# Optimization experiments

Hardware: AMD Instinct MI355X
Metric: run time of the kernel (lower is better)

Reference implementation:

```python
import jax, jax.numpy as jnp
import numpy as np

TEMP = 0.1
EPS = 1e-8


def setup_inputs() -> dict:
    key = jax.random.key(0)
    k1, k2, k3, k4 = jax.random.split(key, 4)
    b, c, H, W = 2, 64, 80, 80
    proj_main = jax.random.normal(k1, (b, c, H, W), dtype=jnp.float32)
    proj_ema = jax.random.normal(k2, (b, c, H, W), dtype=jnp.float32)
    label_main = jax.random.randint(k3, (b, H, W), 0, 2, dtype=jnp.int32)
    label_ema = jax.random.randint(k4, (b, H, W), 0, 2, dtype=jnp.int32)
    return {"proj_main": proj_main, "proj_ema": proj_ema,
            "label_main": label_main, "label_ema": label_ema,
            "patch_num": 8}


def reference(proj_main, proj_ema, label_main, label_ema, patch_num):
    # Labels / FC fractions are computed in the original forward but never
    # consumed by ContrastiveLoss, so they do not affect the output.
    # All patches have equal size h*w, so the per-patch-mean-of-means equals
    # the global mean over all b*H*W anchors; negative column ordering is
    # irrelevant to the row-wise logsumexp. Hence the nested loop fuses to:
    b, c, H, W = proj_main.shape
    A = jnp.transpose(proj_main, (0, 2, 3, 1)).reshape(-1, c)  # (N, c) anchors
    E = jnp.transpose(proj_ema, (0, 2, 3, 1)).reshape(-1, c)   # (N, c) ema feats
    pos = jnp.sum(A * E, axis=-1) / TEMP                       # (N,)
    neg = jnp.einsum('nc,mc->nm', A, E) / TEMP                 # (N, N)
    full = jnp.concatenate([pos[:, None], neg], axis=1)        # (N, N+1)
    m = jnp.max(full, axis=1)                                  # (N,) row max
    denom = jnp.sum(jnp.exp(full - m[:, None]), axis=1)        # (N,)
    loss = -jnp.log(jnp.exp(pos - m) / (denom + EPS) + EPS)
    return jnp.mean(loss)
```

## Files before the change

kernel.cpp:

```cpp
#include <hip/hip_runtime.h>
#include <stdint.h>

#define NA 12800
#define CCH 64
#define TB 2048
#define NSEG 200
#define SC 14.4269504088896340736f
#define MARGIN 41.0f
#define FLOOR_LOSS 18.420680743952367f
#define MAXF 6400
#define NPARTS 20
#define SGMAX 8

typedef __attribute__((ext_vector_type(4))) float f32x4;
typedef __attribute__((ext_vector_type(8))) short s16x8;

#if __has_builtin(__builtin_amdgcn_exp2f)
#define EXP2(x) __builtin_amdgcn_exp2f(x)
#else
#define EXP2(x) exp2f(x)
#endif

__device__ __forceinline__ uint16_t f2bf(float x) {
  uint32_t u = __float_as_uint(x);
  return (uint16_t)((u + 0x7FFFu + ((u >> 16) & 1u)) >> 16);
}

__global__ __launch_bounds__(256) void prepscreen_k(const float* __restrict__ pm,
                                                    const float* __restrict__ pe,
                                                    char* __restrict__ A,
                                                    char* __restrict__ E,
                                                    float* __restrict__ P2,
                                                    int* __restrict__ wl,
                                                    int* __restrict__ fidx,
                                                    int* __restrict__ bcnt,
                                                    int* __restrict__ done) {
  if (blockIdx.x == 0 && threadIdx.x == 0) *done = 0;
  const int blk = blockIdx.x;
  const int tid = threadIdx.x;
  const int lane = tid & 63;
  const int wid = tid >> 6;
  const int l15 = lane & 15, lhi = lane >> 4;
  const f32x4 z4 = (f32x4){0.f, 0.f, 0.f, 0.f};

  __shared__ float pp[4][64];
  __shared__ int flg[64];

  {
    const int n = blk * 64 + lane;
    const int b = n / 6400, p = n - b * 6400;
    const float* am = pm + (size_t)b * CCH * 6400 + p;
    const float* ae = pe + (size_t)b * CCH * 6400 + p;
    char* abase = A + (size_t)(n >> 4) * TB + (n & 15) * 16;
    char* ebase = E + (size_t)(n >> 4) * TB + (n & 15) * 16;

    float pos = 0.0f;
#pragma unroll
    for (int cg2 = 0; cg2 < 2; ++cg2) {
      const int cg = wid * 2 + cg2;
      s16x8 ah, eh;
#pragma unroll
      for (int j = 0; j < 8; ++j) {
        int chn = cg * 8 + j;
        float a = am[(size_t)chn * 6400];
        float e = ae[(size_t)chn * 6400];
        pos = fmaf(a, e, pos);
        ah[j] = (short)f2bf(a * SC);
        eh[j] = (short)f2bf(e);
      }
      const int off = (cg >> 2) * 1024 + (cg & 3) * 256;
      *(s16x8*)(abase + off) = ah;
      *(s16x8*)(ebase + off) = eh;
    }
    pp[wid][lane] = pos;
    __syncthreads();
    if (wid == 0)
      P2[n] = ((pp[0][lane] + pp[1][lane]) + (pp[2][lane] + pp[3][lane])) * SC;
    __syncthreads();
  }

  {
    s16x8 af[2];
#pragma unroll
    for (int ks = 0; ks < 2; ++ks)
      af[ks] = *(const s16x8*)(A + (size_t)(blk * 4 + wid) * TB + ks * 1024 + lane * 16);

    s16x8 b[8][2];
#pragma unroll
    for (int t = 0; t < 8; ++t) {
      const size_t base_t = (t >= 4) ? ((size_t)CCH * 6400 + (t * 1600 - 6400))
                                     : (size_t)(t * 1600);
#pragma unroll
      for (int kh = 0; kh < 2; ++kh) {
#pragma unroll
        for (int j = 0; j < 8; ++j) {
          int ch = kh * 32 + lhi * 8 + j;
          float e = pe[base_t + (size_t)ch * 6400 + l15];
          b[t][kh][j] = (short)f2bf(e);
        }
      }
    }

    float m4[4];
#pragma unroll
    for (int i = 0; i < 4; ++i) m4[i] = -__builtin_inff();

#pragma unroll
    for (int t = 0; t < 8; ++t) {
      f32x4 a_ = __builtin_amdgcn_mfma_f32_16x16x32_bf16(af[0], b[t][0], z4, 0, 0, 0);
      a_ = __builtin_amdgcn_mfma_f32_16x16x32_bf16(af[1], b[t][1], a_, 0, 0, 0);
#pragma unroll
      for (int j = 0; j < 4; ++j) m4[j] = fmaxf(m4[j], a_[j]);
    }
#pragma unroll
    for (int j = 0; j < 4; ++j) {
      float m = m4[j];
#pragma unroll
      for (int mask = 1; mask < 16; mask <<= 1) m = fmaxf(m, __shfl_xor(m, mask));
      m4[j] = m;
    }
    if (l15 == 0) {
#pragma unroll
      for (int j = 0; j < 4; ++j) {
        int rl = wid * 16 + lhi * 4 + j;
        flg[rl] = !(m4[j] > P2[blk * 64 + rl] + MARGIN);
      }
    }
  }
  __syncthreads();

  if (tid < 64) {
    int f = flg[tid];
    unsigned long long mask = __ballot(f != 0);
    int idx = (int)__popcll(mask & ((1ull << lane) - 1));
    if (f) wl[blk * 64 + idx] = blk * 64 + tid;
    fidx[blk * 64 + tid] = f ? idx : -1;
    if (tid == 0) bcnt[blk] = (int)__popcll(mask);
  }
}

__device__ __forceinline__ int slot2row(const int* __restrict__ spfx,
                                        const int* __restrict__ wl, int sl) {
  int lo = 0, hi = NSEG - 1;
  while (lo < hi) {
    int mid = (lo + hi + 1) >> 1;
    if (spfx[mid] <= sl) lo = mid; else hi = mid - 1;
  }
  return wl[lo * 64 + (sl - spfx[lo])];
}

__global__ __launch_bounds__(256, 2) void exact_k(const char* __restrict__ A,
                                                  const char* __restrict__ E,
                                                  const int* __restrict__ wl,
                                                  const int* __restrict__ bcnt,
                                                  float* __restrict__ Pm,
                                                  float* __restrict__ Ps) {
  const int part = blockIdx.x >> 3;
  const int sg0 = blockIdx.x & 7;
  const int tid = threadIdx.x;
  const int lane = tid & 63;
  const int wid = tid >> 6;
  const int wm = wid >> 1, wn = wid & 1;
  const int l15 = lane & 15, lhi = lane >> 4;
  const f32x4 z4 = (f32x4){0.f, 0.f, 0.f, 0.f};

  __shared__ int scan[256];
  __shared__ int spfx[NSEG + 1];
  scan[tid] = (tid < NSEG) ? bcnt[tid] : 0;
  __syncthreads();
#pragma unroll
  for (int off = 1; off < 256; off <<= 1) {
    int v = (tid >= off) ? scan[tid - off] : 0;
    __syncthreads();
    scan[tid] += v;
    __syncthreads();
  }
  if (tid == 0) spfx[0] = 0;
  if (tid < NSEG) spfx[tid + 1] = scan[tid];
  __syncthreads();
  int nr = spfx[NSEG]; if (nr > MAXF) nr = MAXF;

  for (int sg = sg0; sg * 64 < nr; sg += SGMAX) {
    const int sbase = sg * 64 + wm * 32;
    s16x8 af[2][2];
#pragma unroll
    for (int rt = 0; rt < 2; ++rt) {
      int sl = sbase + rt * 16 + l15;
      int n = slot2row(spfx, wl, sl < nr ? sl : 0);
#pragma unroll
      for (int ks = 0; ks < 2; ++ks)
        af[rt][ks] = *(const s16x8*)(A + (size_t)(n >> 4) * TB + ks * 1024 + lhi * 256 + (n & 15) * 16);
    }

    float m8[8], s8[8];
#pragma unroll
    for (int i = 0; i < 8; ++i) { m8[i] = -__builtin_inff(); s8[i] = 0.0f; }

    for (int c = 0; c < 5; ++c) {
      s16x8 b[4][2];
#pragma unroll
      for (int ct = 0; ct < 4; ++ct)
#pragma unroll
        for (int kh = 0; kh < 2; ++kh)
          b[ct][kh] = *(const s16x8*)(E + (size_t)(part * 40 + c * 8 + wn * 4 + ct) * TB + kh * 1024 + lane * 16);

      f32x4 acc[2][4];
#pragma unroll
      for (int ct = 0; ct < 4; ++ct)
#pragma unroll
        for (int rt = 0; rt < 2; ++rt) {
          acc[rt][ct] = __builtin_amdgcn_mfma_f32_16x16x32_bf16(af[rt][0], b[ct][0], z4, 0, 0, 0);
          acc[rt][ct] = __builtin_amdgcn_mfma_f32_16x16x32_bf16(af[rt][1], b[ct][1], acc[rt][ct], 0, 0, 0);
        }

#pragma unroll
      for (int rt = 0; rt < 2; ++rt)
#pragma unroll
        for (int j = 0; j < 4; ++j) {
          const int ri = rt * 4 + j;
          float v0 = acc[rt][0][j], v1 = acc[rt][1][j], v2 = acc[rt][2][j], v3 = acc[rt][3][j];
          float vm = fmaxf(fmaxf(fmaxf(v0, v1), v2), v3);
          float mo = m8[ri];
          float mn = fmaxf(mo, vm);
          float t = (EXP2(v0 - mn) + EXP2(v1 - mn)) + (EXP2(v2 - mn) + EXP2(v3 - mn));
          s8[ri] = fmaf(s8[ri], EXP2(mo - mn), t);
          m8[ri] = mn;
        }
    }

#pragma unroll
    for (int ri = 0; ri < 8; ++ri) {
      float m = m8[ri], s = s8[ri];
#pragma unroll
      for (int mask = 1; mask < 16; mask <<= 1) {
        float mo = __shfl_xor(m, mask);
        float so = __shfl_xor(s, mask);
        float mn = fmaxf(m, mo);
        s = s * EXP2(m - mn) + so * EXP2(mo - mn);
        m = mn;
      }
      m8[ri] = m; s8[ri] = s;
    }
    if (l15 == 0) {
#pragma unroll
      for (int rt = 0; rt < 2; ++rt)
#pragma unroll
        for (int j = 0; j < 4; ++j) {
          int slot = sbase + rt * 16 + lhi * 4 + j;
          if (slot < nr) {
            Pm[(size_t)part * MAXF + slot] = m8[rt * 4 + j];
            Ps[(size_t)part * MAXF + slot] = s8[rt * 4 + j];
          }
        }
    }
  }
}

__global__ __launch_bounds__(256) void final_k(const float* __restrict__ P2,
                                               const int* __restrict__ fidx,
                                               const int* __restrict__ bcnt,
                                               const float* __restrict__ Pm,
                                               const float* __restrict__ Ps,
                                               float* __restrict__ bsum,
                                               int* __restrict__ done,
                                               float* __restrict__ out) {
  const int tid = threadIdx.x;
  __shared__ int scan[256];
  __shared__ float red[4];
  __shared__ int lastf;

  scan[tid] = (tid < NSEG) ? bcnt[tid] : 0;
  __syncthreads();
#pragma unroll
  for (int off = 1; off < 256; off <<= 1) {
    int v = (tid >= off) ? scan[tid - off] : 0;
    __syncthreads();
    scan[tid] += v;
    __syncthreads();
  }

  int n = blockIdx.x * 256 + tid;
  int fl = fidx[n];
  float loss = FLOOR_LOSS;
  if (fl >= 0) {
    int g = n >> 6;
    int fi = (g ? scan[g - 1] : 0) + fl;
    if (fi < MAXF) {
      float m = -__builtin_inff(), s = 0.0f;
#pragma unroll
      for (int p = 0; p < NPARTS; ++p) {
        float mi = Pm[(size_t)p * MAXF + fi];
        float si = Ps[(size_t)p * MAXF + fi];
        float mn = fmaxf(m, mi);
        s = s * EXP2(m - mn) + si * EXP2(mi - mn);
        m = mn;
      }
      float p2 = P2[n];
      float mn = fmaxf(m, p2);
      float e = EXP2(p2 - mn);
      float sf = s * EXP2(m - mn) + e;
      loss = -logf(e / (sf + 1e-8f) + 1e-8f);
    }
  }

  float v = loss;
#pragma unroll
  for (int off = 32; off > 0; off >>= 1) v += __shfl_down(v, off);
  if ((tid & 63) == 0) red[tid >> 6] = v;
  __syncthreads();
  if (tid == 0) {
    bsum[blockIdx.x] = (red[0] + red[1]) + (red[2] + red[3]);
    __threadfence();
    lastf = (atomicAdd(done, 1) == (NA / 256) - 1);
  }
  __syncthreads();
  if (lastf && tid < 64) {
    __threadfence();
    float t = (tid < NA / 256) ? bsum[tid] : 0.0f;
#pragma unroll
    for (int off = 32; off > 0; off >>= 1) t += __shfl_down(t, off);
    if (tid == 0) out[0] = t * (1.0f / (float)NA);
  }
}

extern "C" void kernel_launch(void* const* d_in, const int* in_sizes, int n_in,
                              void* d_out, int out_size, void* d_ws, size_t ws_size,
                              hipStream_t stream) {
  const float* pm = (const float*)d_in[0];
  const float* pe = (const float*)d_in[1];

  char* ws = (char*)d_ws;
  char* Abuf  = ws;
  char* Ebuf  = ws + 1638400;
  float* P2   = (float*)(ws + 3276800);
  float* Pm   = (float*)(ws + 3328000);
  float* Ps   = (float*)(ws + 3840000);
  int*   wl   = (int*)  (ws + 4352000);
  int*   fidx = (int*)  (ws + 4403200);
  int*   bcnt = (int*)  (ws + 4454400);
  int*   done = (int*)  (ws + 4455200);
  float* bsum = (float*)(ws + 4455232);

  prepscreen_k<<<NA / 64, 256, 0, stream>>>(pm, pe, Abuf, Ebuf, P2, wl, fidx, bcnt, done);
  exact_k<<<NPARTS * SGMAX, 256, 0, stream>>>(Abuf, Ebuf, wl, bcnt, Pm, Ps);
  final_k<<<NA / 256, 256, 0, stream>>>(P2, fidx, bcnt, Pm, Ps, bsum, done, (float*)d_out);
}
```

Measured before the change: 30.51 us.

## Fuse final loss reduction into exact kernel via last-block pattern

Removes the separate final_k launch. The last exact_k block to finish, detected with an atomic counter, merges the partial max/sum values over the flagged rows, looks each row's P2 up through a binary search in the prefix table, and adds the floor loss for all unflagged rows in closed form. The aim is to save one kernel launch plus the fidx and bsum traffic. The trade-off is a serial tail: one 256-thread block now processes up to 6400 rows, each with 20 partials.

```diff
diff --git a/kernel.cpp b/kernel.cpp
--- a/kernel.cpp
+++ b/kernel.cpp
@@ -11,6 +11,7 @@
 #define MAXF 6400
 #define NPARTS 20
 #define SGMAX 8
+#define EXB (NPARTS * SGMAX)
 
 typedef __attribute__((ext_vector_type(4))) float f32x4;
 typedef __attribute__((ext_vector_type(8))) short s16x8;
@@ -32,7 +33,6 @@
                                                     char* __restrict__ E,
                                                     float* __restrict__ P2,
                                                     int* __restrict__ wl,
-                                                    int* __restrict__ fidx,
                                                     int* __restrict__ bcnt,
                                                     int* __restrict__ done) {
   if (blockIdx.x == 0 && threadIdx.x == 0) *done = 0;
@@ -134,7 +134,6 @@
     unsigned long long mask = __ballot(f != 0);
     int idx = (int)__popcll(mask & ((1ull << lane) - 1));
     if (f) wl[blk * 64 + idx] = blk * 64 + tid;
-    fidx[blk * 64 + tid] = f ? idx : -1;
     if (tid == 0) bcnt[blk] = (int)__popcll(mask);
   }
 }
@@ -153,8 +152,11 @@
                                                   const char* __restrict__ E,
                                                   const int* __restrict__ wl,
                                                   const int* __restrict__ bcnt,
+                                                  const float* __restrict__ P2,
                                                   float* __restrict__ Pm,
-                                                  float* __restrict__ Ps) {
+                                                  float* __restrict__ Ps,
+                                                  int* __restrict__ done,
+                                                  float* __restrict__ out) {
   const int part = blockIdx.x >> 3;
   const int sg0 = blockIdx.x & 7;
   const int tid = threadIdx.x;
@@ -166,6 +168,8 @@
 
   __shared__ int scan[256];
   __shared__ int spfx[NSEG + 1];
+  __shared__ float red[4];
+  __shared__ int lastf;
   scan[tid] = (tid < NSEG) ? bcnt[tid] : 0;
   __syncthreads();
 #pragma unroll
@@ -254,72 +258,40 @@
         }
     }
   }
-}
-
-__global__ __launch_bounds__(256) void final_k(const float* __restrict__ P2,
-                                               const int* __restrict__ fidx,
-                                               const int* __restrict__ bcnt,
-                                               const float* __restrict__ Pm,
-                                               const float* __restrict__ Ps,
-                                               float* __restrict__ bsum,
-                                               int* __restrict__ done,
-                                               float* __restrict__ out) {
-  const int tid = threadIdx.x;
-  __shared__ int scan[256];
-  __shared__ float red[4];
-  __shared__ int lastf;
-
-  scan[tid] = (tid < NSEG) ? bcnt[tid] : 0;
-  __syncthreads();
-#pragma unroll
-  for (int off = 1; off < 256; off <<= 1) {
-    int v = (tid >= off) ? scan[tid - off] : 0;
-    __syncthreads();
-    scan[tid] += v;
-    __syncthreads();
-  }
-
-  int n = blockIdx.x * 256 + tid;
-  int fl = fidx[n];
-  float loss = FLOOR_LOSS;
-  if (fl >= 0) {
-    int g = n >> 6;
-    int fi = (g ? scan[g - 1] : 0) + fl;
-    if (fi < MAXF) {
-      float m = -__builtin_inff(), s = 0.0f;
-#pragma unroll
-      for (int p = 0; p < NPARTS; ++p) {
-        float mi = Pm[(size_t)p * MAXF + fi];
-        float si = Ps[(size_t)p * MAXF + fi];
-        float mn = fmaxf(m, mi);
-        s = s * EXP2(m - mn) + si * EXP2(mi - mn);
-        m = mn;
-      }
-      float p2 = P2[n];
-      float mn = fmaxf(m, p2);
-      float e = EXP2(p2 - mn);
-      float sf = s * EXP2(m - mn) + e;
-      loss = -logf(e / (sf + 1e-8f) + 1e-8f);
-    }
-  }
-
-  float v = loss;
-#pragma unroll
-  for (int off = 32; off > 0; off >>= 1) v += __shfl_down(v, off);
-  if ((tid & 63) == 0) red[tid >> 6] = v;
-  __syncthreads();
+
   if (tid == 0) {
-    bsum[blockIdx.x] = (red[0] + red[1]) + (red[2] + red[3]);
     __threadfence();
-    lastf = (atomicAdd(done, 1) == (NA / 256) - 1);
-  }
-  __syncthreads();
-  if (lastf && tid < 64) {
-    __threadfence();
-    float t = (tid < NA / 256) ? bsum[tid] : 0.0f;
-#pragma unroll
-    for (int off = 32; off > 0; off >>= 1) t += __shfl_down(t, off);
-    if (tid == 0) out[0] = t * (1.0f / (float)NA);
+    lastf = (atomicAdd(done, 1) == EXB - 1);
+  }
+  __syncthreads();
+  if (!lastf) return;
+  __threadfence();
+
+  float accl = 0.0f;
+  for (int slot = tid; slot < nr; slot += 256) {
+    float m = -__builtin_inff(), s = 0.0f;
+#pragma unroll
+    for (int p = 0; p < NPARTS; ++p) {
+      float mi = Pm[(size_t)p * MAXF + slot];
+      float si = Ps[(size_t)p * MAXF + slot];
+      float mn = fmaxf(m, mi);
+      s = s * EXP2(m - mn) + si * EXP2(mi - mn);
+      m = mn;
+    }
+    float p2 = P2[slot2row(spfx, wl, slot)];
+    float mn = fmaxf(m, p2);
+    float e = EXP2(p2 - mn);
+    float sf = s * EXP2(m - mn) + e;
+    accl += -logf(e / (sf + 1e-8f) + 1e-8f);
+  }
+#pragma unroll
+  for (int off = 32; off > 0; off >>= 1) accl += __shfl_down(accl, off);
+  if ((tid & 63) == 0) red[tid >> 6] = accl;
+  __syncthreads();
+  if (tid == 0) {
+    float total = (red[0] + red[1]) + (red[2] + red[3]) +
+                  (float)(NA - nr) * FLOOR_LOSS;
+    out[0] = total * (1.0f / (float)NA);
   }
 }
 
@@ -336,12 +308,9 @@
   float* Pm   = (float*)(ws + 3328000);
   float* Ps   = (float*)(ws + 3840000);
   int*   wl   = (int*)  (ws + 4352000);
-  int*   fidx = (int*)  (ws + 4403200);
-  int*   bcnt = (int*)  (ws + 4454400);
-  int*   done = (int*)  (ws + 4455200);
-  float* bsum = (float*)(ws + 4455232);
-
-  prepscreen_k<<<NA / 64, 256, 0, stream>>>(pm, pe, Abuf, Ebuf, P2, wl, fidx, bcnt, done);
-  exact_k<<<NPARTS * SGMAX, 256, 0, stream>>>(Abuf, Ebuf, wl, bcnt, Pm, Ps);
-  final_k<<<NA / 256, 256, 0, stream>>>(P2, fidx, bcnt, Pm, Ps, bsum, done, (float*)d_out);
-}
+  int*   bcnt = (int*)  (ws + 4403200);
+  int*   done = (int*)  (ws + 4404000);
+
+  prepscreen_k<<<NA / 64, 256, 0, stream>>>(pm, pe, Abuf, Ebuf, P2, wl, bcnt, done);
+  exact_k<<<EXB, 256, 0, stream>>>(Abuf, Ebuf, wl, bcnt, P2, Pm, Ps, done, (float*)d_out);
+}
```

Result: no change. 30.07 us (-1.4%).
